# Performance work log

Hardware: AMD Instinct MI355X
Metric: run time of the kernel (lower is better)

## Reference

```python
import jax, jax.numpy as jnp
import numpy as np

B, T, D, H, O = 1024, 2048, 13, 128, 2


def setup_inputs() -> dict:
    key = jax.random.key(0)
    k1, k2, k3, k4 = jax.random.split(key, 4)
    xs = jax.random.normal(k1, (B, T, D), dtype=jnp.float32)
    # nn.Linear(in, out, bias=False) weights: [out, in]
    W_in = jax.random.normal(k2, (H, D), dtype=jnp.float32) / np.sqrt(D).astype(np.float32)
    W_h = jax.random.normal(k3, (H, H), dtype=jnp.float32) / np.sqrt(H).astype(np.float32)
    W_out = jax.random.normal(k4, (O, H), dtype=jnp.float32) / np.sqrt(H).astype(np.float32)
    return {"xs": xs, "W_in": W_in, "W_h": W_h, "W_out": W_out}


def reference(xs, W_in, W_h, W_out):
    # Vanilla hardtanh RNN, h0 = 0 (first step y = hardtanh(in_h(x)) == hardtanh(in_h(x) + W_h @ 0)).
    # Precompute all input projections in one big GEMM: [B, T, H]
    pre = jnp.einsum('btd,hd->bth', xs, W_in)

    def step(h, xh_t):  # h: [B, H], xh_t: [B, H]
        h = jnp.clip(xh_t + h @ W_h.T, -1.0, 1.0)  # F.hardtanh
        return h, None

    h0 = jnp.zeros((xs.shape[0], W_in.shape[0]), dtype=xs.dtype)
    hT, _ = jax.lax.scan(step, h0, jnp.swapaxes(pre, 0, 1))  # scan over time
    # Only the final hidden state per sequence is projected to the output.
    return hT @ W_out.T  # [B, O]
```

## Files before the change

### kernel.cpp

```cpp
#include <hip/hip_runtime.h>
#include <stdint.h>


#define RNN_B 1024
#define RNN_T 2048
#define RNN_D 13
#define RNN_H 128
#define RNN_O 2

#define NB 16
#define NWAVE 4
#define NTHR (NWAVE * 64)
#define ROWS 136

using f32x4 = __attribute__((ext_vector_type(4))) float;
using v8s   = __attribute__((ext_vector_type(8))) short;

__device__ __forceinline__ short f2bf(float f) {
    union { float f; uint32_t u; } c; c.f = f;
    uint32_t u = c.u + 0x7fffu + ((c.u >> 16) & 1u);
    return (short)(u >> 16);
}
__device__ __forceinline__ float bf2fs(short s) {
    union { uint32_t u; float f; } c; c.u = ((uint32_t)(uint16_t)s) << 16;
    return c.f;
}
__device__ __forceinline__ float bitf(uint32_t u) {
    union { uint32_t u; float f; } c; c.u = u; return c.f;
}
__device__ __forceinline__ uint32_t cvtpk(float a, float b) {
    uint32_t r;
    asm("v_cvt_pk_bf16_f32 %0, %1, %2" : "=v"(r) : "v"(a), "v"(b));
    return r;
}
__device__ __forceinline__ v8s pack4(uint32_t a, uint32_t b, uint32_t c, uint32_t d) {
    union { uint32_t u[4]; v8s s; } z;
    z.u[0] = a; z.u[1] = b; z.u[2] = c; z.u[3] = d; return z.s;
}
__device__ __forceinline__ float clamp1(float v) {
    return __builtin_amdgcn_fmed3f(v, -1.0f, 1.0f);
}

__device__ __forceinline__ void barrier_lgkm() {
    __builtin_amdgcn_sched_barrier(0);
    asm volatile("s_waitcnt lgkmcnt(0)" ::: "memory");
    __builtin_amdgcn_s_barrier();
    asm volatile("" ::: "memory");
    __builtin_amdgcn_sched_barrier(0);
}

#define MFMA(a, b, c) __builtin_amdgcn_mfma_f32_16x16x32_bf16((a), (b), (c), 0, 0, 0)

#define STEP(CUR, NXT, X0, X1, X2, X3, TPF)                                      \
  do {                                                                           \
           \
    v8s bh1 = *(const v8s*)&Hhi[CUR][n][ktq1 + g8];                              \
    v8s bl1 = *(const v8s*)&Hlo[CUR][n][ktq1 + g8];                              \
    v8s bh2 = *(const v8s*)&Hhi[CUR][n][ktq2 + g8];                              \
    v8s bl2 = *(const v8s*)&Hlo[CUR][n][ktq2 + g8];                              \
    v8s bh3 = *(const v8s*)&Hhi[CUR][n][ktq3 + g8];                              \
    v8s bl3 = *(const v8s*)&Hlo[CUR][n][ktq3 + g8];                              \
                                \
    float m0 = X0, m1 = X1, m2 = X2, m3 = X3;                                    \
    if (g == 3) { m1 = 0.0f; m2 = 0.0f; m3 = 0.0f; }                             \
    uint32_t xh01 = cvtpk(m0, m1), xh23 = cvtpk(m2, m3);                         \
    float q0 = m0 - bitf(xh01 << 16);                                            \
    float q1 = m1 - bitf(xh01 & 0xffff0000u);                                    \
    float q2 = m2 - bitf(xh23 << 16);                                            \
    float q3 = m3 - bitf(xh23 & 0xffff0000u);                                    \
    uint32_t xl01 = cvtpk(q0, q1), xl23 = cvtpk(q2, q3);                         \
    v8s xh = pack4(xh01, xh23, 0u, 0u);                                          \
    v8s xl = pack4(xl01, xl23, 0u, 0u);                                          \
               \
    f32x4 Z = {0.f, 0.f, 0.f, 0.f};                                              \
    f32x4 A1 = MFMA(whiA[4], xh, Z);                                             \
    f32x4 B1 = MFMA(whiB[4], xh, Z);                                             \
    f32x4 A2 = MFMA(whiA[4], xl, Z);                                             \
    f32x4 B2 = MFMA(whiB[4], xl, Z);                                             \
    f32x4 A3 = MFMA(wloA[4], xh, Z);                                             \
    f32x4 B3 = MFMA(wloB[4], xh, Z);                                             \
    A1 = MFMA(whiA[0], selfBh, A1);                                              \
    B1 = MFMA(whiB[0], selfBh, B1);                                              \
    A2 = MFMA(whiA[0], selfBl, A2);                                              \
    B2 = MFMA(whiB[0], selfBl, B2);                                              \
    A3 = MFMA(wloA[0], selfBh, A3);                                              \
    B3 = MFMA(wloB[0], selfBh, B3);                                              \
             \
    if ((TPF) < RNN_T) {                                                         \
      const float* xp = xrow + (size_t)(TPF) * RNN_D;                            \
      X0 = xp[d0]; X1 = xp[d1]; X2 = xp[d2]; X3 = xp[d3];                        \
    }                                                                            \
                                 \
    A1 = MFMA(whiA[1], bh1, A1);                                                 \
    B1 = MFMA(whiB[1], bh1, B1);                                                 \
    A2 = MFMA(whiA[1], bl1, A2);                                                 \
    B2 = MFMA(whiB[1], bl1, B2);                                                 \
    A3 = MFMA(wloA[1], bh1, A3);                                                 \
    B3 = MFMA(wloB[1], bh1, B3);                                                 \
    A1 = MFMA(whiA[2], bh2, A1);                                                 \
    B1 = MFMA(whiB[2], bh2, B1);                                                 \
    A2 = MFMA(whiA[2], bl2, A2);                                                 \
    B2 = MFMA(whiB[2], bl2, B2);                                                 \
    A3 = MFMA(wloA[2], bh2, A3);                                                 \
    B3 = MFMA(wloB[2], bh2, B3);                                                 \
    A1 = MFMA(whiA[3], bh3, A1);                                                 \
    A2 = MFMA(whiA[3], bl3, A2);                                                 \
    A3 = MFMA(wloA[3], bh3, A3);                                                 \
                               \
    float v0 = clamp1(A1[0] + A2[0] + A3[0]);                                    \
    float v1 = clamp1(A1[1] + A2[1] + A3[1]);                                    \
    float v2 = clamp1(A1[2] + A2[2] + A3[2]);                                    \
    float v3 = clamp1(A1[3] + A2[3] + A3[3]);                                    \
    B1 = MFMA(whiB[3], bh3, B1);                                                 \
    B2 = MFMA(whiB[3], bl3, B2);                                                 \
    B3 = MFMA(wloB[3], bh3, B3);                                                 \
    uint32_t h01A = cvtpk(v0, v1), h23A = cvtpk(v2, v3);                         \
    float p0 = v0 - bitf(h01A << 16);                                            \
    float p1 = v1 - bitf(h01A & 0xffff0000u);                                    \
    float p2 = v2 - bitf(h23A << 16);                                            \
    float p3 = v3 - bitf(h23A & 0xffff0000u);                                    \
    uint32_t l01A = cvtpk(p0, p1), l23A = cvtpk(p2, p3);                         \
             \
    {                                                                            \
      float w0 = clamp1(B1[0] + B2[0] + B3[0]);                                  \
      float w1 = clamp1(B1[1] + B2[1] + B3[1]);                                  \
      float w2 = clamp1(B1[2] + B2[2] + B3[2]);                                  \
      float w3 = clamp1(B1[3] + B2[3] + B3[3]);                                  \
      uint32_t h01B = cvtpk(w0, w1), h23B = cvtpk(w2, w3);                       \
      float r0 = w0 - bitf(h01B << 16);                                          \
      float r1 = w1 - bitf(h01B & 0xffff0000u);                                  \
      float r2 = w2 - bitf(h23B << 16);                                          \
      float r3 = w3 - bitf(h23B & 0xffff0000u);                                  \
      uint32_t l01B = cvtpk(r0, r1), l23B = cvtpk(r2, r3);                       \
      selfBh = pack4(h01A, h23A, h01B, h23B);                                    \
      selfBl = pack4(l01A, l23A, l01B, l23B);                                    \
      *(v8s*)&Hhi[NXT][n][wbase + g8] = selfBh;                                  \
      *(v8s*)&Hlo[NXT][n][wbase + g8] = selfBl;                                  \
    }                                                                            \
    barrier_lgkm();                                                              \
  } while (0)

__global__ __launch_bounds__(NTHR, 1) void rnn_mfma14_kernel(
    const float* __restrict__ xs,
    const float* __restrict__ W_in,
    const float* __restrict__ W_h,
    const float* __restrict__ W_out,
    float* __restrict__ out)
{
    __shared__ __align__(16) short Hhi[2][NB][ROWS];
    __shared__ __align__(16) short Hlo[2][NB][ROWS];

    const int tid  = threadIdx.x;
    const int lane = tid & 63;
    const int wid  = tid >> 6;
    const int n    = lane & 15;
    const int g    = lane >> 4;
    const int g8   = g * 8;
    const int wbase = 32 * wid;
    const int b0   = blockIdx.x * NB;

    const int ktq1 = ((wid + 1) & 3) * 32;
    const int ktq2 = ((wid + 2) & 3) * 32;
    const int ktq3 = ((wid + 3) & 3) * 32;

    const int d0 = (4 * g + 0 > 12) ? 12 : 4 * g + 0;
    const int d1 = (4 * g + 1 > 12) ? 12 : 4 * g + 1;
    const int d2 = (4 * g + 2 > 12) ? 12 : 4 * g + 2;
    const int d3 = (4 * g + 3 > 12) ? 12 : 4 * g + 3;

    v8s whiA[5], wloA[5], whiB[5], wloB[5];
    #pragma unroll
    for (int mi = 0; mi < 2; ++mi) {
        const int row = 16 * (wid * 2 + mi) + n;
        #pragma unroll
        for (int q = 0; q < 4; ++q) {
            const int kt = (wid + q) & 3;
            v8s h8, l8;
            #pragma unroll
            for (int j = 0; j < 4; ++j) {
                const float w1 = W_h[row * RNN_H + 32 * kt + 4 * g + j];
                const float w2 = W_h[row * RNN_H + 32 * kt + 16 + 4 * g + j];
                const short h1 = f2bf(w1);
                const short h2 = f2bf(w2);
                h8[j] = h1; h8[4 + j] = h2;
                l8[j] = f2bf(w1 - bf2fs(h1));
                l8[4 + j] = f2bf(w2 - bf2fs(h2));
            }
            if (mi == 0) { whiA[q] = h8; wloA[q] = l8; }
            else         { whiB[q] = h8; wloB[q] = l8; }
        }
        {
            v8s h8, l8;
            #pragma unroll
            for (int j = 0; j < 4; ++j) {
                const int kx = 4 * g + j;
                const float w1 = (kx < RNN_D) ? W_in[row * RNN_D + kx] : 0.0f;
                const short h1 = f2bf(w1);
                h8[j] = h1; h8[4 + j] = 0;
                l8[j] = f2bf(w1 - bf2fs(h1));
                l8[4 + j] = 0;
            }
            if (mi == 0) { whiA[4] = h8; wloA[4] = l8; }
            else         { whiB[4] = h8; wloB[4] = l8; }
        }
    }

    for (int idx = tid; idx < NB * ROWS; idx += NTHR) {
        (&Hhi[0][0][0])[idx] = 0;
        (&Hlo[0][0][0])[idx] = 0;
    }

    v8s selfBh = {0, 0, 0, 0, 0, 0, 0, 0};
    v8s selfBl = {0, 0, 0, 0, 0, 0, 0, 0};

    const float* xrow = xs + (size_t)(b0 + n) * RNN_T * RNN_D;
    float xa0 = xrow[d0], xa1 = xrow[d1], xa2 = xrow[d2], xa3 = xrow[d3];
    float xb0 = xrow[RNN_D + d0], xb1 = xrow[RNN_D + d1];
    float xb2 = xrow[RNN_D + d2], xb3 = xrow[RNN_D + d3];
    __syncthreads();

    for (int t = 0; t < RNN_T; t += 2) {
        STEP(0, 1, xa0, xa1, xa2, xa3, t + 2);
        STEP(1, 0, xb0, xb1, xb2, xb3, t + 3);
    }

    __syncthreads();

    if (wid == 0 && lane < NB * RNN_O) {
        const int nn = lane & 15;
        const int o  = lane >> 4;
        float acc = 0.0f;
        for (int i = 0; i < RNN_H; ++i) {
            const int pos = 32 * (i >> 5) + 8 * ((i >> 2) & 3)
                          + 4 * ((i >> 4) & 1) + (i & 3);
            const float hv = bf2fs(Hhi[0][nn][pos]) + bf2fs(Hlo[0][nn][pos]);
            acc = fmaf(W_out[o * RNN_H + i], hv, acc);
        }
        out[(size_t)(b0 + nn) * RNN_O + o] = acc;
    }
}

extern "C" void kernel_launch(void* const* d_in, const int* in_sizes, int n_in,
                              void* d_out, int out_size, void* d_ws, size_t ws_size,
                              hipStream_t stream) {
    const float* xs    = (const float*)d_in[0];
    const float* W_in  = (const float*)d_in[1];
    const float* W_h   = (const float*)d_in[2];
    const float* W_out = (const float*)d_in[3];
    float* out = (float*)d_out;

    rnn_mfma14_kernel<<<RNN_B / NB, NTHR, 0, stream>>>(xs, W_in, W_h, W_out, out);
}
```

Measured before the change: 1.236 ms.

## XOR-swizzle hidden-state LDS layout and reorder MFMA chains per half

Replaces the padded [NB][136] shared-memory layout for the hidden state with an unpadded [NB*128] layout. The 16-byte chunk index is XOR-swizzled with the batch row, which is meant to avoid LDS bank conflicts on the v8s reads and writes. It also reorders the MFMA sequence so all A-half accumulations run first and the B-half chain overlaps with the A-half clamp and bf16 split, shortening the serial tail before the barrier. The final output readback is adjusted to the swizzled addressing.

```diff
diff --git a/kernel.cpp b/kernel.cpp
--- a/kernel.cpp
+++ b/kernel.cpp
@@ -11,7 +11,6 @@
 #define NB 16
 #define NWAVE 4
 #define NTHR (NWAVE * 64)
-#define ROWS 136
 
 using f32x4 = __attribute__((ext_vector_type(4))) float;
 using v8s   = __attribute__((ext_vector_type(8))) short;
@@ -53,13 +52,13 @@
 
 #define STEP(CUR, NXT, X0, X1, X2, X3, TPF)                                      \
   do {                                                                           \
-           \
-    v8s bh1 = *(const v8s*)&Hhi[CUR][n][ktq1 + g8];                              \
-    v8s bl1 = *(const v8s*)&Hlo[CUR][n][ktq1 + g8];                              \
-    v8s bh2 = *(const v8s*)&Hhi[CUR][n][ktq2 + g8];                              \
-    v8s bl2 = *(const v8s*)&Hlo[CUR][n][ktq2 + g8];                              \
-    v8s bh3 = *(const v8s*)&Hhi[CUR][n][ktq3 + g8];                              \
-    v8s bl3 = *(const v8s*)&Hlo[CUR][n][ktq3 + g8];                              \
+                     \
+    v8s bh1 = *(const v8s*)&Hhi[CUR][off1];                                      \
+    v8s bl1 = *(const v8s*)&Hlo[CUR][off1];                                      \
+    v8s bh2 = *(const v8s*)&Hhi[CUR][off2];                                      \
+    v8s bl2 = *(const v8s*)&Hlo[CUR][off2];                                      \
+    v8s bh3 = *(const v8s*)&Hhi[CUR][off3];                                      \
+    v8s bl3 = *(const v8s*)&Hlo[CUR][off3];                                      \
                                 \
     float m0 = X0, m1 = X1, m2 = X2, m3 = X3;                                    \
     if (g == 3) { m1 = 0.0f; m2 = 0.0f; m3 = 0.0f; }                             \
@@ -71,56 +70,55 @@
     uint32_t xl01 = cvtpk(q0, q1), xl23 = cvtpk(q2, q3);                         \
     v8s xh = pack4(xh01, xh23, 0u, 0u);                                          \
     v8s xl = pack4(xl01, xl23, 0u, 0u);                                          \
-               \
+                    \
     f32x4 Z = {0.f, 0.f, 0.f, 0.f};                                              \
     f32x4 A1 = MFMA(whiA[4], xh, Z);                                             \
-    f32x4 B1 = MFMA(whiB[4], xh, Z);                                             \
     f32x4 A2 = MFMA(whiA[4], xl, Z);                                             \
-    f32x4 B2 = MFMA(whiB[4], xl, Z);                                             \
     f32x4 A3 = MFMA(wloA[4], xh, Z);                                             \
-    f32x4 B3 = MFMA(wloB[4], xh, Z);                                             \
     A1 = MFMA(whiA[0], selfBh, A1);                                              \
-    B1 = MFMA(whiB[0], selfBh, B1);                                              \
     A2 = MFMA(whiA[0], selfBl, A2);                                              \
-    B2 = MFMA(whiB[0], selfBl, B2);                                              \
     A3 = MFMA(wloA[0], selfBh, A3);                                              \
-    B3 = MFMA(wloB[0], selfBh, B3);                                              \
              \
     if ((TPF) < RNN_T) {                                                         \
       const float* xp = xrow + (size_t)(TPF) * RNN_D;                            \
       X0 = xp[d0]; X1 = xp[d1]; X2 = xp[d2]; X3 = xp[d3];                        \
     }                                                                            \
-                                 \
     A1 = MFMA(whiA[1], bh1, A1);                                                 \
-    B1 = MFMA(whiB[1], bh1, B1);                                                 \
     A2 = MFMA(whiA[1], bl1, A2);                                                 \
-    B2 = MFMA(whiB[1], bl1, B2);                                                 \
     A3 = MFMA(wloA[1], bh1, A3);                                                 \
-    B3 = MFMA(wloB[1], bh1, B3);                                                 \
     A1 = MFMA(whiA[2], bh2, A1);                                                 \
-    B1 = MFMA(whiB[2], bh2, B1);                                                 \
     A2 = MFMA(whiA[2], bl2, A2);                                                 \
-    B2 = MFMA(whiB[2], bl2, B2);                                                 \
     A3 = MFMA(wloA[2], bh2, A3);                                                 \
-    B3 = MFMA(wloB[2], bh2, B3);                                                 \
     A1 = MFMA(whiA[3], bh3, A1);                                                 \
     A2 = MFMA(whiA[3], bl3, A2);                                                 \
     A3 = MFMA(wloA[3], bh3, A3);                                                 \
-                               \
+                \
+    f32x4 B1 = MFMA(whiB[4], xh, Z);                                             \
+    f32x4 B2 = MFMA(whiB[4], xl, Z);                                             \
+    f32x4 B3 = MFMA(wloB[4], xh, Z);                                             \
+    B1 = MFMA(whiB[0], selfBh, B1);                                              \
+    B2 = MFMA(whiB[0], selfBl, B2);                                              \
+    B3 = MFMA(wloB[0], selfBh, B3);                                              \
     float v0 = clamp1(A1[0] + A2[0] + A3[0]);                                    \
     float v1 = clamp1(A1[1] + A2[1] + A3[1]);                                    \
     float v2 = clamp1(A1[2] + A2[2] + A3[2]);                                    \
     float v3 = clamp1(A1[3] + A2[3] + A3[3]);                                    \
-    B1 = MFMA(whiB[3], bh3, B1);                                                 \
-    B2 = MFMA(whiB[3], bl3, B2);                                                 \
-    B3 = MFMA(wloB[3], bh3, B3);                                                 \
+    B1 = MFMA(whiB[1], bh1, B1);                                                 \
+    B2 = MFMA(whiB[1], bl1, B2);                                                 \
+    B3 = MFMA(wloB[1], bh1, B3);                                                 \
     uint32_t h01A = cvtpk(v0, v1), h23A = cvtpk(v2, v3);                         \
     float p0 = v0 - bitf(h01A << 16);                                            \
     float p1 = v1 - bitf(h01A & 0xffff0000u);                                    \
     float p2 = v2 - bitf(h23A << 16);                                            \
     float p3 = v3 - bitf(h23A & 0xffff0000u);                                    \
+    B1 = MFMA(whiB[2], bh2, B1);                                                 \
+    B2 = MFMA(whiB[2], bl2, B2);                                                 \
+    B3 = MFMA(wloB[2], bh2, B3);                                                 \
     uint32_t l01A = cvtpk(p0, p1), l23A = cvtpk(p2, p3);                         \
-             \
+    B1 = MFMA(whiB[3], bh3, B1);                                                 \
+    B2 = MFMA(whiB[3], bl3, B2);                                                 \
+    B3 = MFMA(wloB[3], bh3, B3);                                                 \
+        \
     {                                                                            \
       float w0 = clamp1(B1[0] + B2[0] + B3[0]);                                  \
       float w1 = clamp1(B1[1] + B2[1] + B3[1]);                                  \
@@ -134,34 +132,33 @@
       uint32_t l01B = cvtpk(r0, r1), l23B = cvtpk(r2, r3);                       \
       selfBh = pack4(h01A, h23A, h01B, h23B);                                    \
       selfBl = pack4(l01A, l23A, l01B, l23B);                                    \
-      *(v8s*)&Hhi[NXT][n][wbase + g8] = selfBh;                                  \
-      *(v8s*)&Hlo[NXT][n][wbase + g8] = selfBl;                                  \
+      *(v8s*)&Hhi[NXT][offw] = selfBh;                                           \
+      *(v8s*)&Hlo[NXT][offw] = selfBl;                                           \
     }                                                                            \
     barrier_lgkm();                                                              \
   } while (0)
 
-__global__ __launch_bounds__(NTHR, 1) void rnn_mfma14_kernel(
+__global__ __launch_bounds__(NTHR, 1) void rnn_mfma18_kernel(
     const float* __restrict__ xs,
     const float* __restrict__ W_in,
     const float* __restrict__ W_h,
     const float* __restrict__ W_out,
     float* __restrict__ out)
 {
-    __shared__ __align__(16) short Hhi[2][NB][ROWS];
-    __shared__ __align__(16) short Hlo[2][NB][ROWS];
+    __shared__ __align__(16) short Hhi[2][NB * 128];
+    __shared__ __align__(16) short Hlo[2][NB * 128];
 
     const int tid  = threadIdx.x;
     const int lane = tid & 63;
     const int wid  = tid >> 6;
     const int n    = lane & 15;
     const int g    = lane >> 4;
-    const int g8   = g * 8;
-    const int wbase = 32 * wid;
     const int b0   = blockIdx.x * NB;
 
-    const int ktq1 = ((wid + 1) & 3) * 32;
-    const int ktq2 = ((wid + 2) & 3) * 32;
-    const int ktq3 = ((wid + 3) & 3) * 32;
+    const int off1 = n * 128 + (((((wid + 1) & 3) << 2) + g) ^ n) * 8;
+    const int off2 = n * 128 + (((((wid + 2) & 3) << 2) + g) ^ n) * 8;
+    const int off3 = n * 128 + (((((wid + 3) & 3) << 2) + g) ^ n) * 8;
+    const int offw = n * 128 + (((wid << 2) + g) ^ n) * 8;
 
     const int d0 = (4 * g + 0 > 12) ? 12 : 4 * g + 0;
     const int d1 = (4 * g + 1 > 12) ? 12 : 4 * g + 1;
@@ -205,9 +202,9 @@
         }
     }
 
-    for (int idx = tid; idx < NB * ROWS; idx += NTHR) {
-        (&Hhi[0][0][0])[idx] = 0;
-        (&Hlo[0][0][0])[idx] = 0;
+    for (int idx = tid; idx < NB * 128; idx += NTHR) {
+        Hhi[0][idx] = 0;
+        Hlo[0][idx] = 0;
     }
 
     v8s selfBh = {0, 0, 0, 0, 0, 0, 0, 0};
@@ -233,7 +230,8 @@
         for (int i = 0; i < RNN_H; ++i) {
             const int pos = 32 * (i >> 5) + 8 * ((i >> 2) & 3)
                           + 4 * ((i >> 4) & 1) + (i & 3);
-            const float hv = bf2fs(Hhi[0][nn][pos]) + bf2fs(Hlo[0][nn][pos]);
+            const int adr = nn * 128 + ((pos >> 3) ^ nn) * 8 + (pos & 7);
+            const float hv = bf2fs(Hhi[0][adr]) + bf2fs(Hlo[0][adr]);
             acc = fmaf(W_out[o * RNN_H + i], hv, acc);
         }
         out[(size_t)(b0 + nn) * RNN_O + o] = acc;
@@ -249,5 +247,5 @@
     const float* W_out = (const float*)d_in[3];
     float* out = (float*)d_out;
 
-    rnn_mfma14_kernel<<<RNN_B / NB, NTHR, 0, stream>>>(xs, W_in, W_h, W_out, out);
-}
+    rnn_mfma18_kernel<<<RNN_B / NB, NTHR, 0, stream>>>(xs, W_in, W_h, W_out, out);
+}
```

Result: no change. 1.217 ms (-1.6%).
